# Kernel tuning notes

Hardware: AMD Instinct MI355X
Metric: run time of the kernel (lower is better)

Reference implementation:

```python
import jax, jax.numpy as jnp
import numpy as np

VEC_DIM = 4096
N_PAIRS = 4096
N_QUERIES = 4096


def _round_pow2(length: int) -> int:
    if length <= 0:
        return 1
    return 1 << (length - 1).bit_length()


def _pad_pow2(x):
    d = x.shape[-1]
    p = _round_pow2(d)
    if p > d:
        x = jnp.pad(x, [(0, 0)] * (x.ndim - 1) + [(0, p - d)])
    return x


def setup_inputs() -> dict:
    key = jax.random.key(0)
    k1, k2, k3 = jax.random.split(key, 3)
    keys = jax.random.normal(k1, (N_PAIRS, VEC_DIM), dtype=jnp.float32)
    values = jax.random.normal(k2, (N_PAIRS, VEC_DIM), dtype=jnp.float32)
    query_keys = jax.random.normal(k3, (N_QUERIES, VEC_DIM), dtype=jnp.float32)
    return {"keys": keys, "values": values, "query_keys": query_keys}


def reference(keys, values, query_keys):
    """store(keys, values) into a superposed trace, then retrieve(query_keys).

    Faithful batched form of the torch module: by linearity of FFT/IFFT,
    memory = sum_i IFFT(FFT(k_i) * FFT(v_i)).real is computed with one
    batched FFT pair instead of a Python loop over pairs.
    """
    d = keys.shape[-1]
    # --- store: memory = sum_i twist_merge(k_i, v_i) ---
    fk = jnp.fft.fft(_pad_pow2(keys), axis=-1)          # [N, P] complex
    fv = jnp.fft.fft(_pad_pow2(values), axis=-1)        # [N, P] complex
    bound = jnp.fft.ifft(fk * fv, axis=-1).real[..., :d]  # [N, D]
    memory = jnp.sum(bound, axis=0)                     # [D]

    # --- retrieve: twist_split(memory, q) = IFFT(FFT(memory)*conj(FFT(q))).real ---
    fm = jnp.fft.fft(_pad_pow2(memory), axis=-1)        # [P] complex
    fq = jnp.fft.fft(_pad_pow2(query_keys), axis=-1)    # [Q, P] complex
    retrieved = jnp.fft.ifft(fm[None, :] * jnp.conj(fq), axis=-1).real[..., :d]
    return retrieved  # [Q, D]
```

## Files before the change

### kernel.cpp

```cpp
#include <hip/hip_runtime.h>
#include <stdint.h>

#define DD 4096
#define NPAIR 4096
#define NQUERY 4096
#define PPB 4

#define SLOT2(i) ((i) + ((((i) >> 5)) << 1))

#define LBAR() do { asm volatile("s_waitcnt lgkmcnt(0)" ::: "memory");        \
                    __builtin_amdgcn_s_barrier();                             \
                    asm volatile("" ::: "memory"); } while (0)

template <int INV>
static __device__ __forceinline__ void fft16(float* zr, float* zi) {
    const float K1 = 0.92387953251128674f;
    const float S1 = 0.38268343236508978f;
    const float C2 = 0.70710678118654752f;
    float gr[16], gi[16];
    #pragma unroll
    for (int n2 = 0; n2 < 4; ++n2) {
        const float x0r = zr[n2],      x0i = zi[n2];
        const float x1r = zr[4 + n2],  x1i = zi[4 + n2];
        const float x2r = zr[8 + n2],  x2i = zi[8 + n2];
        const float x3r = zr[12 + n2], x3i = zi[12 + n2];
        const float s02r = x0r + x2r, s02i = x0i + x2i;
        const float d02r = x0r - x2r, d02i = x0i - x2i;
        const float s13r = x1r + x3r, s13i = x1i + x3i;
        const float d13r = x1r - x3r, d13i = x1i - x3i;
        gr[0 * 4 + n2] = s02r + s13r; gi[0 * 4 + n2] = s02i + s13i;
        gr[2 * 4 + n2] = s02r - s13r; gi[2 * 4 + n2] = s02i - s13i;
        if (!INV) {
            gr[1 * 4 + n2] = d02r + d13i; gi[1 * 4 + n2] = d02i - d13r;
            gr[3 * 4 + n2] = d02r - d13i; gi[3 * 4 + n2] = d02i + d13r;
        } else {
            gr[1 * 4 + n2] = d02r - d13i; gi[1 * 4 + n2] = d02i + d13r;
            gr[3 * 4 + n2] = d02r + d13i; gi[3 * 4 + n2] = d02i - d13r;
        }
    }
#define TW16(K, N, WR, WI) do {                                              \
        const float wr_ = (WR), wi_ = INV ? -(WI) : (WI);                    \
        const float xr_ = gr[(K) * 4 + (N)], xi_ = gi[(K) * 4 + (N)];        \
        gr[(K) * 4 + (N)] = xr_ * wr_ - xi_ * wi_;                           \
        gi[(K) * 4 + (N)] = xr_ * wi_ + xi_ * wr_; } while (0)
    TW16(1, 1, K1, -S1);  TW16(1, 2, C2, -C2);   TW16(1, 3, S1, -K1);
    TW16(2, 1, C2, -C2);  TW16(2, 2, 0.f, -1.f); TW16(2, 3, -C2, -C2);
    TW16(3, 1, S1, -K1);  TW16(3, 2, -C2, -C2);  TW16(3, 3, -K1, S1);
#undef TW16
    #pragma unroll
    for (int k1 = 0; k1 < 4; ++k1) {
        const float x0r = gr[k1 * 4 + 0], x0i = gi[k1 * 4 + 0];
        const float x1r = gr[k1 * 4 + 1], x1i = gi[k1 * 4 + 1];
        const float x2r = gr[k1 * 4 + 2], x2i = gi[k1 * 4 + 2];
        const float x3r = gr[k1 * 4 + 3], x3i = gi[k1 * 4 + 3];
        const float s02r = x0r + x2r, s02i = x0i + x2i;
        const float d02r = x0r - x2r, d02i = x0i - x2i;
        const float s13r = x1r + x3r, s13i = x1i + x3i;
        const float d13r = x1r - x3r, d13i = x1i - x3i;
        zr[k1]      = s02r + s13r; zi[k1]      = s02i + s13i;
        zr[k1 + 8]  = s02r - s13r; zi[k1 + 8]  = s02i - s13i;
        if (!INV) {
            zr[k1 + 4]  = d02r + d13i; zi[k1 + 4]  = d02i - d13r;
            zr[k1 + 12] = d02r - d13i; zi[k1 + 12] = d02i + d13r;
        } else {
            zr[k1 + 4]  = d02r - d13i; zi[k1 + 4]  = d02i + d13r;
            zr[k1 + 12] = d02r + d13i; zi[k1 + 12] = d02i - d13r;
        }
    }
}

static __device__ __forceinline__ void twiddle_chain(float* zr, float* zi,
                                                     float br, float bi) {
    float cr = br, ci = bi;
    #pragma unroll
    for (int k = 1; k < 16; ++k) {
        const float xr = zr[k], xi = zi[k];
        zr[k] = xr * cr - xi * ci;
        zi[k] = xr * ci + xi * cr;
        if (k < 15) {
            const float nr = cr * br - ci * bi;
            const float ni = cr * bi + ci * br;
            cr = nr; ci = ni;
        }
    }
}

template <int INV, int WB3>
static __device__ void fft4096z(float* xr, float* xi, float* zr, float* zi,
                                float b1r, float b1i, float b2r, float b2i,
                                int tid) {
    fft16<INV>(zr, zi);
    twiddle_chain(zr, zi, b1r, b1i);
    #pragma unroll
    for (int k = 0; k < 16; ++k) {
        const int a = SLOT2(k * 256 + tid);
        xr[a] = zr[k]; xi[a] = zi[k];
    }
    __syncthreads();
    const int base2 = (tid >> 4) * 256 + (tid & 15);
    #pragma unroll
    for (int m = 0; m < 16; ++m) {
        const int a = SLOT2(base2 + m * 16);
        zr[m] = xr[a]; zi[m] = xi[a];
    }
    fft16<INV>(zr, zi);
    twiddle_chain(zr, zi, b2r, b2i);
    #pragma unroll
    for (int j = 0; j < 16; ++j) {
        const int a = SLOT2(base2 + j * 16);
        xr[a] = zr[j]; xi[a] = zi[j];
    }
    __syncthreads();
    const int base3 = (tid >> 4) * 256 + (tid & 15) * 16;
    #pragma unroll
    for (int m = 0; m < 16; m += 2) {
        const int a = SLOT2(base3 + m);
        const float2 vr = *(const float2*)&xr[a];
        const float2 vi = *(const float2*)&xi[a];
        zr[m] = vr.x; zr[m + 1] = vr.y;
        zi[m] = vi.x; zi[m + 1] = vi.y;
    }
    fft16<INV>(zr, zi);
    if (WB3) {
        __syncthreads();
        const int ob = (tid >> 4) + (tid & 15) * 16;
        #pragma unroll
        for (int j2 = 0; j2 < 16; ++j2) {
            const int a = SLOT2(ob + j2 * 256);
            xr[a] = zr[j2]; xi[a] = zi[j2];
        }
        __syncthreads();
    }
}

template <int INV>
static __device__ void fft4096s(float* xr, float* xi, float* zr, float* zi,
                                float b1r, float b1i, float b2r, float b2i,
                                int tid) {
    fft16<INV>(zr, zi);
    twiddle_chain(zr, zi, b1r, b1i);
    #pragma unroll
    for (int k = 0; k < 16; ++k) {
        const int a = SLOT2(k * 256 + tid);
        xr[a] = zr[k]; xi[a] = zi[k];
    }
    LBAR();
    const int base2 = (tid >> 4) * 256 + (tid & 15);
    #pragma unroll
    for (int m = 0; m < 16; ++m) {
        const int a = SLOT2(base2 + m * 16);
        zr[m] = xr[a]; zi[m] = xi[a];
    }
    fft16<INV>(zr, zi);
    twiddle_chain(zr, zi, b2r, b2i);
    #pragma unroll
    for (int j = 0; j < 16; ++j) {
        const int a = SLOT2(base2 + j * 16);
        xr[a] = zr[j]; xi[a] = zi[j];
    }
    LBAR();
    const int base3 = (tid >> 4) * 256 + (tid & 15) * 16;
    #pragma unroll
    for (int m = 0; m < 16; m += 2) {
        const int a = SLOT2(base3 + m);
        const float2 vr = *(const float2*)&xr[a];
        const float2 vi = *(const float2*)&xi[a];
        zr[m] = vr.x; zr[m + 1] = vr.y;
        zi[m] = vi.x; zi[m + 1] = vi.y;
    }
    fft16<INV>(zr, zi);
}

__global__ __launch_bounds__(256) void store_kernel(
    const float* __restrict__ keys, const float* __restrict__ values,
    float* __restrict__ Are, float* __restrict__ Aim) {
    __shared__ float xr[4352], xi[4352];
    const int tid = (int)threadIdx.x;

    float b1r, b1i, b2r, b2i;
    {
        const float a1 = -6.2831853071795864769f * (float)tid / 4096.f;
        const float a2 = -6.2831853071795864769f * (float)(tid & 15) / 256.f;
        sincosf(a1, &b1i, &b1r);
        sincosf(a2, &b2i, &b2r);
    }

    float aAr[16], aAi[16];
    #pragma unroll
    for (int r = 0; r < 16; ++r) { aAr[r] = 0.f; aAi[r] = 0.f; }

    const int pair0 = (int)blockIdx.x * PPB;
    float4 ka[4], va[4];
    {
        const float* kp = keys + (size_t)pair0 * DD;
        const float* vp = values + (size_t)pair0 * DD;
        #pragma unroll
        for (int q = 0; q < 4; ++q) {
            ka[q] = ((const float4*)kp)[tid + 256 * q];
            va[q] = ((const float4*)vp)[tid + 256 * q];
        }
    }

    #pragma unroll 1
    for (int p = 0; p < PPB; ++p) {
        LBAR();
        #pragma unroll
        for (int q = 0; q < 4; ++q) {
            const int j = (tid + 256 * q) * 4;
            const int a = SLOT2(j);
            *(float2*)&xr[a]     = make_float2(ka[q].x, ka[q].y);
            *(float2*)&xr[a + 2] = make_float2(ka[q].z, ka[q].w);
            *(float2*)&xi[a]     = make_float2(va[q].x, va[q].y);
            *(float2*)&xi[a + 2] = make_float2(va[q].z, va[q].w);
        }
        if (p + 1 < PPB) {
            const float* kp = keys + (size_t)(pair0 + p + 1) * DD;
            const float* vp = values + (size_t)(pair0 + p + 1) * DD;
            #pragma unroll
            for (int q = 0; q < 4; ++q) {
                ka[q] = ((const float4*)kp)[tid + 256 * q];
                va[q] = ((const float4*)vp)[tid + 256 * q];
            }
        }
        LBAR();
        float zr[16], zi[16];
        #pragma unroll
        for (int n = 0; n < 16; ++n) {
            const int a = SLOT2(n * 256 + tid);
            zr[n] = xr[a]; zi[n] = xi[a];
        }
        fft4096s<0>(xr, xi, zr, zi, b1r, b1i, b2r, b2i, tid);
        #pragma unroll
        for (int j2 = 0; j2 < 16; ++j2) {
            aAr[j2] += zr[j2] * zr[j2] - zi[j2] * zi[j2];
            aAi[j2] += 2.f * zr[j2] * zi[j2];
        }
    }
    LBAR();
    const int ob = (tid >> 4) + (tid & 15) * 16;
    #pragma unroll
    for (int j2 = 0; j2 < 16; ++j2) {
        const int a = SLOT2(ob + j2 * 256);
        xr[a] = aAr[j2]; xi[a] = aAi[j2];
    }
    LBAR();
    #pragma unroll
    for (int r = 0; r < 16; ++r) {
        const int f = tid + 256 * r;
        const int a = SLOT2(f);
        atomicAdd(&Are[f], xr[a]);
        atomicAdd(&Aim[f], xi[a]);
    }
}

__global__ __launch_bounds__(256) void retrieve_kernel(
    const float* __restrict__ queries, const float* __restrict__ Are,
    const float* __restrict__ Aim, float* __restrict__ out) {
    __shared__ float xr[4352], xi[4352];
    const int tid = (int)threadIdx.x;

    float b1r, b1i, b2r, b2i;
    {
        const float a1 = -6.2831853071795864769f * (float)tid / 4096.f;
        const float a2 = -6.2831853071795864769f * (float)(tid & 15) / 256.f;
        sincosf(a1, &b1i, &b1r);
        sincosf(a2, &b2i, &b2r);
    }

    const int q0 = (int)blockIdx.x * 2, q1 = q0 + 1;
    const float* r0 = queries + (size_t)q0 * DD;
    const float* r1 = queries + (size_t)q1 * DD;
    float zr[16], zi[16];
    #pragma unroll
    for (int n = 0; n < 16; ++n) {
        zr[n] = r0[n * 256 + tid];
        zi[n] = r1[n * 256 + tid];
    }
    fft4096z<0, 1>(xr, xi, zr, zi, b1r, b1i, b2r, b2i, tid);

    float zmr[16], zmi[16], fmr[16], fmi[16];
    #pragma unroll
    for (int r = 0; r < 16; ++r) {
        const int f = tid + 256 * r;
        const int fn = (DD - f) & (DD - 1);
        zmr[r] = xr[SLOT2(fn)]; zmi[r] = xi[SLOT2(fn)];
        const float pr = Are[f],  pi_ = Aim[f];
        const float qr = Are[fn], qi_ = Aim[fn];
        fmr[r] = 0.25f * (pi_ + qi_);
        fmi[r] = -0.25f * (pr - qr);
    }
    __syncthreads();
    #pragma unroll
    for (int r = 0; r < 16; ++r) {
        const int f = tid + 256 * r;
        const int a = SLOT2(f);
        xr[a] = fmr[r] * zmr[r] - fmi[r] * zmi[r];
        xi[a] = fmr[r] * zmi[r] + fmi[r] * zmr[r];
    }
    __syncthreads();
    #pragma unroll
    for (int n = 0; n < 16; ++n) {
        const int a = SLOT2(n * 256 + tid);
        zr[n] = xr[a]; zi[n] = xi[a];
    }
    fft4096z<1, 1>(xr, xi, zr, zi, b1r, -b1i, b2r, -b2i, tid);

    const float sc = 1.f / 4096.f;
    float* o0 = out + (size_t)q0 * DD;
    float* o1 = out + (size_t)q1 * DD;
    #pragma unroll
    for (int q = 0; q < 4; ++q) {
        const int j = (tid + 256 * q) * 4;
        const int a = SLOT2(j);
        const float2 r01 = *(const float2*)&xr[a];
        const float2 r23 = *(const float2*)&xr[a + 2];
        const float2 i01 = *(const float2*)&xi[a];
        const float2 i23 = *(const float2*)&xi[a + 2];
        float4 v0, v1;
        v0.x = r01.x * sc; v0.y = r01.y * sc; v0.z = r23.x * sc; v0.w = r23.y * sc;
        v1.x = i01.x * sc; v1.y = i01.y * sc; v1.z = i23.x * sc; v1.w = i23.y * sc;
        ((float4*)o0)[tid + 256 * q] = v0;
        ((float4*)o1)[tid + 256 * q] = v1;
    }
}

extern "C" void kernel_launch(void* const* d_in, const int* in_sizes, int n_in,
                              void* d_out, int out_size, void* d_ws, size_t ws_size,
                              hipStream_t stream) {
    const float* keys    = (const float*)d_in[0];
    const float* values  = (const float*)d_in[1];
    const float* queries = (const float*)d_in[2];
    float* out = (float*)d_out;
    char* ws = (char*)d_ws;

    float* Are = (float*)ws;
    float* Aim = (float*)(ws + 16384);

    hipMemsetAsync(Are, 0, 2 * DD * sizeof(float), stream);

    store_kernel<<<NPAIR / PPB, 256, 0, stream>>>(keys, values, Are, Aim);
    retrieve_kernel<<<NQUERY / 2, 256, 0, stream>>>(queries, Are, Aim, out);
}
```

Before: 90.85 us.

## Merge four store groups per block and pre-reduce in LDS before atomics

The store kernel now runs 1024-thread blocks made of four independent 256-thread groups, each with its own LDS slice and processing four pairs. The four group accumulators are summed in shared memory before the global atomicAdds, which cuts the atomic count by four. The cost is 139 KB of LDS per block, which limits occupancy to one block per CU. Block-wide barriers now also synchronize all four groups together.

```diff
diff --git a/kernel.cpp b/kernel.cpp
--- a/kernel.cpp
+++ b/kernel.cpp
@@ -4,7 +4,6 @@
 #define DD 4096
 #define NPAIR 4096
 #define NQUERY 4096
-#define PPB 4
 
 #define SLOT2(i) ((i) + ((((i) >> 5)) << 1))
 
@@ -171,11 +170,15 @@
     fft16<INV>(zr, zi);
 }
 
-__global__ __launch_bounds__(256) void store_kernel(
+__global__ __launch_bounds__(1024) void store_kernel(
     const float* __restrict__ keys, const float* __restrict__ values,
     float* __restrict__ Are, float* __restrict__ Aim) {
-    __shared__ float xr[4352], xi[4352];
-    const int tid = (int)threadIdx.x;
+    __shared__ float xr[4 * 4352], xi[4 * 4352];
+    const int tid1 = (int)threadIdx.x;
+    const int g = tid1 >> 8;
+    const int tid = tid1 & 255;
+    float* xrg = xr + g * 4352;
+    float* xig = xi + g * 4352;
 
     float b1r, b1i, b2r, b2i;
     {
@@ -189,7 +192,7 @@
     #pragma unroll
     for (int r = 0; r < 16; ++r) { aAr[r] = 0.f; aAi[r] = 0.f; }
 
-    const int pair0 = (int)blockIdx.x * PPB;
+    const int pair0 = (int)blockIdx.x * 16 + g * 4;
     float4 ka[4], va[4];
     {
         const float* kp = keys + (size_t)pair0 * DD;
@@ -202,18 +205,18 @@
     }
 
     #pragma unroll 1
-    for (int p = 0; p < PPB; ++p) {
+    for (int p = 0; p < 4; ++p) {
         LBAR();
         #pragma unroll
         for (int q = 0; q < 4; ++q) {
             const int j = (tid + 256 * q) * 4;
             const int a = SLOT2(j);
-            *(float2*)&xr[a]     = make_float2(ka[q].x, ka[q].y);
-            *(float2*)&xr[a + 2] = make_float2(ka[q].z, ka[q].w);
-            *(float2*)&xi[a]     = make_float2(va[q].x, va[q].y);
-            *(float2*)&xi[a + 2] = make_float2(va[q].z, va[q].w);
-        }
-        if (p + 1 < PPB) {
+            *(float2*)&xrg[a]     = make_float2(ka[q].x, ka[q].y);
+            *(float2*)&xrg[a + 2] = make_float2(ka[q].z, ka[q].w);
+            *(float2*)&xig[a]     = make_float2(va[q].x, va[q].y);
+            *(float2*)&xig[a + 2] = make_float2(va[q].z, va[q].w);
+        }
+        if (p + 1 < 4) {
             const float* kp = keys + (size_t)(pair0 + p + 1) * DD;
             const float* vp = values + (size_t)(pair0 + p + 1) * DD;
             #pragma unroll
@@ -227,9 +230,9 @@
         #pragma unroll
         for (int n = 0; n < 16; ++n) {
             const int a = SLOT2(n * 256 + tid);
-            zr[n] = xr[a]; zi[n] = xi[a];
-        }
-        fft4096s<0>(xr, xi, zr, zi, b1r, b1i, b2r, b2i, tid);
+            zr[n] = xrg[a]; zi[n] = xig[a];
+        }
+        fft4096s<0>(xrg, xig, zr, zi, b1r, b1i, b2r, b2i, tid);
         #pragma unroll
         for (int j2 = 0; j2 < 16; ++j2) {
             aAr[j2] += zr[j2] * zr[j2] - zi[j2] * zi[j2];
@@ -241,15 +244,17 @@
     #pragma unroll
     for (int j2 = 0; j2 < 16; ++j2) {
         const int a = SLOT2(ob + j2 * 256);
-        xr[a] = aAr[j2]; xi[a] = aAi[j2];
+        xrg[a] = aAr[j2]; xig[a] = aAi[j2];
     }
     LBAR();
     #pragma unroll
-    for (int r = 0; r < 16; ++r) {
-        const int f = tid + 256 * r;
+    for (int r = 0; r < 4; ++r) {
+        const int f = tid1 + 1024 * r;
         const int a = SLOT2(f);
-        atomicAdd(&Are[f], xr[a]);
-        atomicAdd(&Aim[f], xi[a]);
+        const float sr = xr[a] + xr[4352 + a] + xr[2 * 4352 + a] + xr[3 * 4352 + a];
+        const float si = xi[a] + xi[4352 + a] + xi[2 * 4352 + a] + xi[3 * 4352 + a];
+        atomicAdd(&Are[f], sr);
+        atomicAdd(&Aim[f], si);
     }
 }
 
@@ -338,6 +343,6 @@
 
     hipMemsetAsync(Are, 0, 2 * DD * sizeof(float), stream);
 
-    store_kernel<<<NPAIR / PPB, 256, 0, stream>>>(keys, values, Are, Aim);
+    store_kernel<<<NPAIR / 16, 1024, 0, stream>>>(keys, values, Are, Aim);
     retrieve_kernel<<<NQUERY / 2, 256, 0, stream>>>(queries, Are, Aim, out);
 }
```

Result: slower. 208.0 us (+128.9%).
